# Kernel optimization log

Hardware: AMD Instinct MI355X
Metric: run time of the kernel (lower is better)

## Reference

```python
import jax, jax.numpy as jnp
import numpy as np
from jax import lax

TOP_N = 4
CAT_NUM = 4
IOU_THRESH = 0.25
PAD = 224
OUT_SZ = 224


def _gen_edge_anchors():
    # Faithful port of NTSNet._generate_default_anchor_maps for 448x448 input.
    settings = (
        dict(stride=32, size=48, scale=[2 ** (1.0 / 3.0), 2 ** (2.0 / 3.0)], ar=[0.667, 1, 1.5]),
        dict(stride=64, size=96, scale=[2 ** (1.0 / 3.0), 2 ** (2.0 / 3.0)], ar=[0.667, 1, 1.5]),
        dict(stride=128, size=192, scale=[1, 2 ** (1.0 / 3.0), 2 ** (2.0 / 3.0)], ar=[0.667, 1, 1.5]),
    )
    inp = np.array([448, 448], dtype=np.float32)
    edges = []
    for s in settings:
        stride = s['stride']
        oh, ow = np.ceil(inp / stride).astype(int)
        ostart = stride / 2.0
        oy = np.arange(ostart, ostart + stride * oh, stride, dtype=np.float32).reshape(oh, 1)
        ox = np.arange(ostart, ostart + stride * ow, stride, dtype=np.float32).reshape(1, ow)
        cy = np.broadcast_to(oy, (oh, ow)); cx = np.broadcast_to(ox, (oh, ow))
        for sc in s['scale']:
            for ar in s['ar']:
                h = s['size'] * sc / float(ar) ** 0.5
                w = s['size'] * sc * float(ar) ** 0.5
                e = np.stack([cy - h / 2.0, cx - w / 2.0, cy + h / 2.0, cx + w / 2.0], axis=-1).reshape(-1, 4)
                edges.append(e)
    return np.concatenate(edges, 0).astype(np.float32)

EDGE_ANCHORS = (_gen_edge_anchors() + PAD).astype(np.int32)  # [1614,4] (y0,x0,y1,x1) in padded coords
BOXES_F = jnp.asarray(EDGE_ANCHORS, jnp.float32)
BOXES_I = jnp.asarray(EDGE_ANCHORS, jnp.int32)
AREAS = (BOXES_F[:, 2] - BOXES_F[:, 0]) * (BOXES_F[:, 3] - BOXES_F[:, 1])
N_ANCHORS = EDGE_ANCHORS.shape[0]  # 1614


def _nms_single(scores):
    # Greedy hard NMS: pick top score, suppress IoU >= thresh, repeat TOP_N times.
    def step(valid, _):
        s = jnp.where(valid, scores, -jnp.inf)
        i = jnp.argmax(s)
        b = BOXES_F[i]
        sy = jnp.maximum(BOXES_F[:, 0], b[0]); sx = jnp.maximum(BOXES_F[:, 1], b[1])
        ey = jnp.minimum(BOXES_F[:, 2], b[2]); ex = jnp.minimum(BOXES_F[:, 3], b[3])
        ly = ey - sy; lx = ex - sx
        inter = jnp.where((ly < 0) | (lx < 0), 0.0, ly * lx)
        iou = inter / (AREAS + AREAS[i] - inter)
        return valid & (iou < IOU_THRESH), i
    _, idx = lax.scan(step, jnp.ones((N_ANCHORS,), bool), None, length=TOP_N)
    return idx  # [TOP_N] int


def _crop_resize(img, box):
    # img: [3, 896, 896]; box: int [4] = (y0,x0,y1,x1); bilinear, align_corners=True -> [3,224,224]
    hmax = img.shape[-1] - 1
    y0, x0, y1, x1 = box[0], box[1], box[2], box[3]
    t = jnp.arange(OUT_SZ, dtype=jnp.float32) / (OUT_SZ - 1.0)
    ys = y0.astype(jnp.float32) + t * (y1 - y0 - 1).astype(jnp.float32)
    xs = x0.astype(jnp.float32) + t * (x1 - x0 - 1).astype(jnp.float32)
    yf = jnp.floor(ys); xf = jnp.floor(xs)
    wy = (ys - yf)[None, :, None]; wx = (xs - xf)[None, None, :]
    yl = yf.astype(jnp.int32); yh = jnp.minimum(yl + 1, hmax)
    xl = xf.astype(jnp.int32); xh = jnp.minimum(xl + 1, hmax)
    g = lambda yi, xi: img[:, yi[:, None], xi[None, :]]
    top = g(yl, xl) * (1.0 - wx) + g(yl, xh) * wx
    bot = g(yh, xl) * (1.0 - wx) + g(yh, xh) * wx
    return top * (1.0 - wy) + bot * wy


def _conv(x, w, b, stride, pad):
    y = lax.conv_general_dilated(x, w, (stride, stride), ((pad, pad), (pad, pad)),
                                 dimension_numbers=('NCHW', 'OIHW', 'NCHW'))
    return y + b[None, :, None, None]


def _forward(x, bb_w, bb_b, w1, b1, t1w, t1b, w2, b2, t2w, t2b, w3, b3, t3w, t3b, cw, cb):
    B = x.shape[0]
    backbone = lambda z: jax.nn.relu(_conv(z, bb_w, bb_b, 32, 0))
    raw_pre = backbone(x)  # [B,2048,14,14]
    # Navigator unit
    y1 = jax.nn.relu(_conv(raw_pre, w1, b1, 1, 1))                                  # [B,128,14,14]
    z1 = (jnp.einsum('bchw,oc->bohw', y1, t1w) + t1b[None, :, None, None]).reshape(B, -1)
    y2 = jax.nn.relu(_conv(y1, w2, b2, 2, 1))                                        # [B,128,7,7]
    z2 = (jnp.einsum('bchw,oc->bohw', y2, t2w) + t2b[None, :, None, None]).reshape(B, -1)
    y3 = jax.nn.relu(_conv(y2, w3, b3, 2, 1))                                        # [B,128,4,4]
    z3 = (jnp.einsum('bchw,oc->bohw', y3, t3w) + t3b[None, :, None, None]).reshape(B, -1)
    rpn_score = jnp.concatenate([z1, z2, z3], axis=1)  # [B,1614]
    top_idx = jax.vmap(_nms_single)(rpn_score)          # [B,TOP_N]
    boxes = BOXES_I[top_idx]                            # [B,TOP_N,4]
    x_pad = jnp.pad(x, ((0, 0), (0, 0), (PAD, PAD), (PAD, PAD)))  # [B,3,896,896]
    parts = jax.vmap(lambda img, bs: jax.vmap(lambda b: _crop_resize(img, b))(bs))(x_pad, boxes)
    parts = lax.stop_gradient(parts).reshape(B * TOP_N, 3, OUT_SZ, OUT_SZ)  # .detach() in torch
    part_feat = backbone(parts).mean(axis=(2, 3)).reshape(B, TOP_N, 2048)
    part_feat = part_feat[:, :CAT_NUM].reshape(B, -1)   # [B,8192]
    raw_feat = lax.stop_gradient(raw_pre).mean(axis=(2, 3))  # [B,2048] (detached in torch)
    concat = jnp.concatenate([part_feat, raw_feat], axis=1)  # [B,10240]
    return concat @ cw.T + cb                           # [B,200]


def setup_inputs() -> dict:
    key = jax.random.key(0)
    ks = jax.random.split(key, 12)
    def w(k, shape, fan_in):
        return jax.random.normal(k, shape, jnp.float32) * np.float32(np.sqrt(2.0 / fan_in))
    return {
        'x': jax.random.normal(ks[0], (8, 3, 448, 448), jnp.float32),
        'bb_w': w(ks[1], (2048, 3, 32, 32), 3 * 32 * 32), 'bb_b': jnp.zeros((2048,), jnp.float32),
        'w1': w(ks[2], (128, 2048, 3, 3), 2048 * 9), 'b1': jnp.zeros((128,), jnp.float32),
        't1w': w(ks[3], (6, 128), 128), 't1b': jnp.zeros((6,), jnp.float32),
        'w2': w(ks[4], (128, 128, 3, 3), 128 * 9), 'b2': jnp.zeros((128,), jnp.float32),
        't2w': w(ks[5], (6, 128), 128), 't2b': jnp.zeros((6,), jnp.float32),
        'w3': w(ks[6], (128, 128, 3, 3), 128 * 9), 'b3': jnp.zeros((128,), jnp.float32),
        't3w': w(ks[7], (9, 128), 128), 't3b': jnp.zeros((9,), jnp.float32),
        'cw': w(ks[8], (200, 2048 * (CAT_NUM + 1)), 2048 * (CAT_NUM + 1)),
        'cb': jnp.zeros((200,), jnp.float32),
    }


def reference(x, bb_w, bb_b, w1, b1, t1w, t1b, w2, b2, t2w, t2b, w3, b3, t3w, t3b, cw, cb):
    return _forward(x, bb_w, bb_b, w1, b1, t1w, t1b, w2, b2, t2w, t2b, w3, b3, t3w, t3b, cw, cb)
```

## Files before the change

### kernel.cpp

```cpp
#include <hip/hip_runtime.h>
#include <math.h>


typedef _Float16 h8 __attribute__((ext_vector_type(8)));
typedef float f32x4 __attribute__((ext_vector_type(4)));

#define ASCALE 256.0f
#define WSCALE 16384.0f
#define RSCALE (1.0f / (256.0f * 16384.0f))
#define PSLAB ((size_t)1664 * 2048)

__device__ __forceinline__ void gload16(const void* g, void* l) {
  __builtin_amdgcn_global_load_lds(
      (__attribute__((address_space(1))) void*)(void*)(uintptr_t)g,
      (__attribute__((address_space(3))) void*)l, 16, 0, 0);
}

__device__ void anchors_body(int i, int* anch, float* areas) {
  if (i >= 1614) return;
  int stride, oh, a, pos;
  double size, sc;
  const double C13 = 1.2599210498948732;
  const double C23 = 1.5874010519681994;
  if (i < 1176) {
    stride = 32; size = 48.0; oh = 14; a = i / 196; pos = i % 196;
    sc = (a / 3 == 0) ? C13 : C23;
  } else if (i < 1470) {
    int r = i - 1176; stride = 64; size = 96.0; oh = 7; a = r / 49; pos = r % 49;
    sc = (a / 3 == 0) ? C13 : C23;
  } else {
    int r = i - 1470; stride = 128; size = 192.0; oh = 4; a = r / 16; pos = r % 16;
    int si = a / 3;
    sc = (si == 0) ? 1.0 : ((si == 1) ? C13 : C23);
  }
  int ari = a % 3;
  double ar = (ari == 0) ? 0.667 : ((ari == 1) ? 1.0 : 1.5);
  int gy = pos / oh, gx = pos % oh;
  float cy = 0.5f * (float)stride + (float)(stride * gy);
  float cx = 0.5f * (float)stride + (float)(stride * gx);
  double ss = sqrt(ar);
  double hd = (size * sc) / ss;
  double wd = (size * sc) * ss;
  float hh = (float)(hd * 0.5), wh = (float)(wd * 0.5);
  int y0 = (int)((cy - hh) + 224.0f), x0 = (int)((cx - wh) + 224.0f);
  int y1i = (int)((cy + hh) + 224.0f), x1i = (int)((cx + wh) + 224.0f);
  anch[i * 4 + 0] = y0; anch[i * 4 + 1] = x0;
  anch[i * 4 + 2] = y1i; anch[i * 4 + 3] = x1i;
  areas[i] = (float)(y1i - y0) * (float)(x1i - x0);
}

__global__ __launch_bounds__(256) void prep_small(int* __restrict__ anch,
                                                  float* __restrict__ areas,
                                                  const float* __restrict__ w2,
                                                  float* __restrict__ w2p,
                                                  const float* __restrict__ w3,
                                                  float* __restrict__ w3p) {
  int b = blockIdx.x, t = threadIdx.x;
  if (b < 7) { anchors_body(b * 256 + t, anch, areas); return; }
  const float* src; float* dst; int idx;
  if (b < 7 + 576) { src = w2; dst = w2p; idx = (b - 7) * 256 + t; }
  else             { src = w3; dst = w3p; idx = (b - 583) * 256 + t; }
  if (idx >= 128 * 9 * 128) return;
  int c = idx % 128; int r2 = idx / 128; int tap = r2 % 9; int o = r2 / 9;
  dst[idx] = src[(o * 128 + c) * 9 + tap];
}

__global__ __launch_bounds__(256) void split_w(const float* __restrict__ src,
                                               _Float16* __restrict__ h,
                                               _Float16* __restrict__ l, int n8) {
  int i = blockIdx.x * 256 + threadIdx.x;
  if (i >= n8) return;
  float4 v0 = *(const float4*)(src + (size_t)i * 8);
  float4 v1 = *(const float4*)(src + (size_t)i * 8 + 4);
  float vv[8] = {v0.x, v0.y, v0.z, v0.w, v1.x, v1.y, v1.z, v1.w};
  h8 vh, vl;
#pragma unroll
  for (int j = 0; j < 8; ++j) {
    float s = vv[j] * WSCALE;
    _Float16 a = (_Float16)s;
    vh[j] = a; vl[j] = (_Float16)(s - (float)a);
  }
  *(h8*)(h + (size_t)i * 8) = vh;
  *(h8*)(l + (size_t)i * 8) = vl;
}

__global__ __launch_bounds__(256) void split_w1(const float* __restrict__ w1,
                                                _Float16* __restrict__ h,
                                                _Float16* __restrict__ l) {
  __shared__ float buf[4608];
  int o = blockIdx.x >> 2, ct = (blockIdx.x & 3) * 512;
  const float* src = w1 + (size_t)o * 18432 + (size_t)ct * 9;
  for (int i = threadIdx.x; i < 4608; i += 256) buf[i] = src[i];
  __syncthreads();
  for (int i = threadIdx.x; i < 4608; i += 256) {
    int tap = i / 512, c = i - tap * 512;
    float v = buf[c * 9 + tap] * WSCALE;
    _Float16 a = (_Float16)v;
    size_t o2 = ((size_t)o * 9 + tap) * 2048 + ct + c;
    h[o2] = a; l[o2] = (_Float16)(v - (float)a);
  }
}

__global__ __launch_bounds__(256) void split_x(const float* __restrict__ x,
                                               _Float16* __restrict__ Ah,
                                               _Float16* __restrict__ Al) {
  int i = blockIdx.x * 256 + threadIdx.x;
  if (i >= 1664 * 384) return;
  int kq = i % 384, m = i / 384;
  int k = kq * 8;
  h8 vh = {}, vl = {};
  if (m < 1568) {
    int b = m / 196, pos = m % 196;
    int c = k >> 10, r = (k >> 5) & 31, col = k & 31;
    int py = (pos / 14) * 32 + r, px = (pos % 14) * 32 + col;
    const float* sp2 = x + (((size_t)(b * 3 + c) * 448 + py) * 448 + px);
    float4 v0 = *(const float4*)sp2;
    float4 v1 = *(const float4*)(sp2 + 4);
    float vv[8] = {v0.x, v0.y, v0.z, v0.w, v1.x, v1.y, v1.z, v1.w};
#pragma unroll
    for (int j = 0; j < 8; ++j) {
      float s = vv[j] * ASCALE;
      _Float16 a = (_Float16)s;
      vh[j] = a; vl[j] = (_Float16)(s - (float)a);
    }
  }
  *(h8*)(Ah + (size_t)m * 3072 + k) = vh;
  *(h8*)(Al + (size_t)m * 3072 + k) = vl;
}

__global__ __launch_bounds__(256) void gemm_bb_mfma(
    const _Float16* __restrict__ Ah, const _Float16* __restrict__ Al,
    const _Float16* __restrict__ Bh, const _Float16* __restrict__ Bl,
    float* __restrict__ P) {
  __shared__ __align__(16) char lds[65536];
  const int t = threadIdx.x;
  const int bid = blockIdx.x + 13 * blockIdx.y;
  const int r = bid >> 3;
  const int m0 = (r >> 1) * 128;
  const int n0 = ((bid & 7) * 2 + (r & 1)) * 128;
  const int kz = blockIdx.z;
  const int lane = t & 63, w = t >> 6;
  const int wm = (w >> 1) * 64, wn = (w & 1) * 64;
  const int lrow = lane & 15, kg = lane >> 4;

  int offA[4], offB[4];
#pragma unroll
  for (int i = 0; i < 4; ++i) {
    int ba = (wm + i * 16 + lrow) * 64 + kg * 16;
    offA[i] = ba ^ (((ba >> 7) & 3) << 4);
    int bb2 = (wn + i * 16 + lrow) * 64 + kg * 16;
    offB[i] = bb2 ^ (((bb2 >> 7) & 3) << 4);
  }
  size_t gAo[2], gBo[2];
  int ldso[2];
#pragma unroll
  for (int e = 0; e < 2; ++e) {
    int p = e * 256 + t;
    int lsl = p ^ ((p >> 3) & 3);
    int row = lsl >> 2, kq = lsl & 3;
    gAo[e] = (size_t)(m0 + row) * 3072 + kq * 8;
    gBo[e] = (size_t)(n0 + row) * 3072 + kq * 8;
    ldso[e] = e * 4096 + (t & 192) * 16;
  }

  auto STAGE = [&](int buf, int k0) {
    char* L = lds + buf * 32768;
#pragma unroll
    for (int e = 0; e < 2; ++e) {
      gload16(Ah + gAo[e] + k0, L + ldso[e]);
      gload16(Al + gAo[e] + k0, L + 8192 + ldso[e]);
      gload16(Bh + gBo[e] + k0, L + 16384 + ldso[e]);
      gload16(Bl + gBo[e] + k0, L + 24576 + ldso[e]);
    }
  };

  f32x4 acc[4][4] = {};
  const int kbeg = kz * 1536, kend = kbeg + 1536;
  STAGE(0, kbeg);
  __syncthreads();
  int cur = 0;
  for (int k0 = kbeg; k0 < kend; k0 += 32) {
    if (k0 + 32 < kend) STAGE(cur ^ 1, k0 + 32);
    const char* L = lds + cur * 32768;
    h8 fah[4], fal[4], fbh[4], fbl[4];
#pragma unroll
    for (int i = 0; i < 4; ++i) {
      fah[i] = *(const h8*)(L + offA[i]);
      fal[i] = *(const h8*)(L + 8192 + offA[i]);
      fbh[i] = *(const h8*)(L + 16384 + offB[i]);
      fbl[i] = *(const h8*)(L + 24576 + offB[i]);
    }
#pragma unroll
    for (int i = 0; i < 4; ++i)
#pragma unroll
      for (int j = 0; j < 4; ++j)
        acc[i][j] = __builtin_amdgcn_mfma_f32_16x16x32_f16(fah[i], fbh[j], acc[i][j], 0, 0, 0);
#pragma unroll
    for (int i = 0; i < 4; ++i)
#pragma unroll
      for (int j = 0; j < 4; ++j)
        acc[i][j] = __builtin_amdgcn_mfma_f32_16x16x32_f16(fah[i], fbl[j], acc[i][j], 0, 0, 0);
#pragma unroll
    for (int i = 0; i < 4; ++i)
#pragma unroll
      for (int j = 0; j < 4; ++j)
        acc[i][j] = __builtin_amdgcn_mfma_f32_16x16x32_f16(fal[i], fbh[j], acc[i][j], 0, 0, 0);
    __syncthreads();
    cur ^= 1;
  }
  float* Pz = P + (size_t)kz * PSLAB;
  const int prow = (lane >> 4) * 4;
#pragma unroll
  for (int i = 0; i < 4; ++i) {
#pragma unroll
    for (int j = 0; j < 4; ++j) {
      int n = n0 + wn + j * 16 + lrow;
#pragma unroll
      for (int r2 = 0; r2 < 4; ++r2) {
        int m = m0 + wm + i * 16 + prow + r2;
        Pz[(size_t)m * 2048 + n] = acc[i][j][r2];
      }
    }
  }
}

__global__ __launch_bounds__(256) void bb_reduce_split(const float* __restrict__ P,
                                                       const float* __restrict__ bias,
                                                       _Float16* __restrict__ h,
                                                       _Float16* __restrict__ l) {
  int idx = blockIdx.x * 256 + threadIdx.x;
  int m = idx >> 8, col = (idx & 255) * 8;
  if (m >= 1664) return;
  size_t o = (size_t)m * 2048 + col;
  if (m >= 1568) {
    h8 z = {};
    *(h8*)(h + o) = z;
    *(h8*)(l + o) = z;
    return;
  }
  h8 vh, vl;
#pragma unroll
  for (int q = 0; q < 2; ++q) {
    float4 s0 = *(const float4*)(P + o + q * 4);
    float4 s1 = *(const float4*)(P + PSLAB + o + q * 4);
    float4 b = *(const float4*)(bias + col + q * 4);
    float v[4];
    v[0] = fmaxf(fmaf(s0.x + s1.x, RSCALE, b.x), 0.f);
    v[1] = fmaxf(fmaf(s0.y + s1.y, RSCALE, b.y), 0.f);
    v[2] = fmaxf(fmaf(s0.z + s1.z, RSCALE, b.z), 0.f);
    v[3] = fmaxf(fmaf(s0.w + s1.w, RSCALE, b.w), 0.f);
#pragma unroll
    for (int j = 0; j < 4; ++j) {
      float s = v[j] * ASCALE;
      _Float16 a = (_Float16)s;
      vh[q * 4 + j] = a; vl[q * 4 + j] = (_Float16)(s - (float)a);
    }
  }
  *(h8*)(h + o) = vh;
  *(h8*)(l + o) = vl;
}

__global__ __launch_bounds__(256) void feat_reduce(const float* __restrict__ P,
                                                   const float* __restrict__ bias,
                                                   float* __restrict__ out,
                                                   int rows) {
  int g = blockIdx.x >> 5, chunk = blockIdx.x & 31;
  int col = chunk * 64 + (threadIdx.x & 63), rl = threadIdx.x >> 6;
  const float* base0 = P + ((size_t)g * rows) * 2048 + col;
  const float* base1 = base0 + PSLAB;
  float bcol = bias[col];
  float s = 0.f;
  for (int r = rl; r < rows; r += 4)
    s += fmaxf(fmaf(base0[(size_t)r * 2048] + base1[(size_t)r * 2048], RSCALE, bcol), 0.f);
  __shared__ float red[4][64];
  red[rl][threadIdx.x & 63] = s;
  __syncthreads();
  if (rl == 0) {
    int c = threadIdx.x & 63;
    out[(size_t)g * 2048 + col] =
        ((red[0][c] + red[1][c]) + (red[2][c] + red[3][c])) / (float)rows;
  }
}

__global__ __launch_bounds__(256) void gemm_nav_mfma(
    const _Float16* __restrict__ Ah, const _Float16* __restrict__ Al,
    const _Float16* __restrict__ Bh, const _Float16* __restrict__ Bl,
    float* __restrict__ part) {
  __shared__ __align__(16) char lds[65536];
  const int t = threadIdx.x;
  const int bid = blockIdx.x + 13 * blockIdx.y;
  const int orig = (bid & 7) * 52 + (bid >> 3);
  const int m0 = (orig % 13) * 128;
  const int sp = orig / 13;
  const int lane = t & 63, w = t >> 6;
  const int wm = (w >> 1) * 64, wn = (w & 1) * 64;
  const int lrow = lane & 15, kg = lane >> 4;

  int offA[4], offB[4];
#pragma unroll
  for (int i = 0; i < 4; ++i) {
    int ba = (wm + i * 16 + lrow) * 64 + kg * 16;
    offA[i] = ba ^ (((ba >> 7) & 3) << 4);
    int bb2 = (wn + i * 16 + lrow) * 64 + kg * 16;
    offB[i] = bb2 ^ (((bb2 >> 7) & 3) << 4);
  }
  size_t gBo[2];
  int ldso[2], akq8[2], ab[2], apy[2], apx[2], amv[2];
#pragma unroll
  for (int e = 0; e < 2; ++e) {
    int p = e * 256 + t;
    int lsl = p ^ ((p >> 3) & 3);
    int row = lsl >> 2, kq = lsl & 3;
    gBo[e] = (size_t)row * 18432 + kq * 8;
    ldso[e] = e * 4096 + (t & 192) * 16;
    int m = m0 + row;
    amv[e] = (m < 1568);
    int b = m / 196, pos = m % 196;
    ab[e] = b; apy[e] = pos / 14; apx[e] = pos % 14;
    akq8[e] = kq * 8;
  }

  auto STAGE = [&](int buf, int k0) {
    const int tap = k0 >> 11;
    const int c = k0 & 2047;
    const int dy = tap / 3 - 1, dx = tap % 3 - 1;
    char* L = lds + buf * 32768;
#pragma unroll
    for (int e = 0; e < 2; ++e) {
      int sy = apy[e] + dy, sx = apx[e] + dx;
      bool ok = amv[e] && ((unsigned)sy < 14u) && ((unsigned)sx < 14u);
      size_t rowi = ok ? (size_t)(ab[e] * 196 + sy * 14 + sx) : (size_t)1600;
      size_t ao = rowi * 2048 + c + akq8[e];
      gload16(Ah + ao, L + ldso[e]);
      gload16(Al + ao, L + 8192 + ldso[e]);
      gload16(Bh + gBo[e] + k0, L + 16384 + ldso[e]);
      gload16(Bl + gBo[e] + k0, L + 24576 + ldso[e]);
    }
  };

  f32x4 acc[4][4] = {};
  const int kbeg = sp * 576, kend = kbeg + 576;
  STAGE(0, kbeg);
  __syncthreads();
  int cur = 0;
  for (int k0 = kbeg; k0 < kend; k0 += 32) {
    if (k0 + 32 < kend) STAGE(cur ^ 1, k0 + 32);
    const char* L = lds + cur * 32768;
    h8 fah[4], fal[4], fbh[4], fbl[4];
#pragma unroll
    for (int i = 0; i < 4; ++i) {
      fah[i] = *(const h8*)(L + offA[i]);
      fal[i] = *(const h8*)(L + 8192 + offA[i]);
      fbh[i] = *(const h8*)(L + 16384 + offB[i]);
      fbl[i] = *(const h8*)(L + 24576 + offB[i]);
    }
#pragma unroll
    for (int i = 0; i < 4; ++i)
#pragma unroll
      for (int j = 0; j < 4; ++j)
        acc[i][j] = __builtin_amdgcn_mfma_f32_16x16x32_f16(fah[i], fbh[j], acc[i][j], 0, 0, 0);
#pragma unroll
    for (int i = 0; i < 4; ++i)
#pragma unroll
      for (int j = 0; j < 4; ++j)
        acc[i][j] = __builtin_amdgcn_mfma_f32_16x16x32_f16(fah[i], fbl[j], acc[i][j], 0, 0, 0);
#pragma unroll
    for (int i = 0; i < 4; ++i)
#pragma unroll
      for (int j = 0; j < 4; ++j)
        acc[i][j] = __builtin_amdgcn_mfma_f32_16x16x32_f16(fal[i], fbh[j], acc[i][j], 0, 0, 0);
    __syncthreads();
    cur ^= 1;
  }
  const int prow = (lane >> 4) * 4;
#pragma unroll
  for (int i = 0; i < 4; ++i) {
#pragma unroll
    for (int j = 0; j < 4; ++j) {
      int n = wn + j * 16 + lrow;
#pragma unroll
      for (int r = 0; r < 4; ++r) {
        int m = m0 + wm + i * 16 + prow + r;
        if (m < 1568)
          part[((size_t)sp * 1568 + m) * 128 + n] = acc[i][j][r] * RSCALE;
      }
    }
  }
}

__global__ __launch_bounds__(256) void y1_reduce(const float* __restrict__ part,
                                                 const float* __restrict__ b1,
                                                 float* __restrict__ y1) {
  int idx = blockIdx.x * 256 + threadIdx.x;
  if (idx >= 1568 * 32) return;
  int o = (idx * 4) & 127;
  float4 s = *(const float4*)(b1 + o);
#pragma unroll
  for (int sp = 0; sp < 32; ++sp) {
    float4 v = *(const float4*)(part + (size_t)sp * 1568 * 128 + (size_t)idx * 4);
    s.x += v.x; s.y += v.y; s.z += v.z; s.w += v.w;
  }
  s.x = fmaxf(s.x, 0.f); s.y = fmaxf(s.y, 0.f);
  s.z = fmaxf(s.z, 0.f); s.w = fmaxf(s.w, 0.f);
  *(float4*)(y1 + (size_t)idx * 4) = s;
}

__global__ __launch_bounds__(256) void conv3x3s2(const float* __restrict__ in,
                                                 const float* __restrict__ wp,
                                                 const float* __restrict__ bias,
                                                 float* __restrict__ out,
                                                 int Hin, int Hout) {
  int idx = blockIdx.x * 256 + threadIdx.x;
  int total = 8 * Hout * Hout * 128;
  if (idx >= total) return;
  int o = idx & 127; int pos = idx >> 7;
  int ox = pos % Hout; int t2 = pos / Hout; int oy = t2 % Hout; int b = t2 / Hout;
  float acc = bias[o];
  for (int dy = 0; dy < 3; ++dy) {
    int iy = 2 * oy - 1 + dy;
    if (iy < 0 || iy >= Hin) continue;
    for (int dx = 0; dx < 3; ++dx) {
      int ix = 2 * ox - 1 + dx;
      if (ix < 0 || ix >= Hin) continue;
      const float* ip = in + ((b * Hin + iy) * Hin + ix) * 128;
      const float* wgt = wp + (o * 9 + dy * 3 + dx) * 128;
#pragma unroll 4
      for (int c = 0; c < 128; c += 4) {
        float4 a = *(const float4*)(ip + c);
        float4 ww = *(const float4*)(wgt + c);
        acc += a.x * ww.x + a.y * ww.y + a.z * ww.z + a.w * ww.w;
      }
    }
  }
  out[idx] = fmaxf(acc, 0.f);
}

__global__ __launch_bounds__(256) void scores_kernel(
    const float* __restrict__ y1, const float* __restrict__ y2,
    const float* __restrict__ y3, const float* __restrict__ t1w,
    const float* __restrict__ t1b, const float* __restrict__ t2w,
    const float* __restrict__ t2b, const float* __restrict__ t3w,
    const float* __restrict__ t3b, float* __restrict__ scores) {
  int idx = blockIdx.x * 256 + threadIdx.x;
  if (idx >= 8 * 1614) return;
  int b = idx / 1614, sI = idx % 1614;
  const float* f; const float* w; float bias;
  if (sI < 1176) {
    int a = sI / 196;
    f = y1 + (b * 196 + (sI % 196)) * 128; w = t1w + a * 128; bias = t1b[a];
  } else if (sI < 1470) {
    int r = sI - 1176; int a = r / 49;
    f = y2 + (b * 49 + (r % 49)) * 128; w = t2w + a * 128; bias = t2b[a];
  } else {
    int r = sI - 1470; int a = r / 16;
    f = y3 + (b * 16 + (r % 16)) * 128; w = t3w + a * 128; bias = t3b[a];
  }
  float acc = 0.f;
  for (int c = 0; c < 128; c += 4) {
    float4 a4 = *(const float4*)(f + c);
    float4 w4 = *(const float4*)(w + c);
    acc += a4.x * w4.x + a4.y * w4.y + a4.z * w4.z + a4.w * w4.w;
  }
  scores[idx] = acc + bias;
}

__global__ __launch_bounds__(256) void nms_kernel(const float* __restrict__ scores,
                                                  const int* __restrict__ anch,
                                                  const float* __restrict__ areas,
                                                  int* __restrict__ boxes) {
  const int b = blockIdx.x, t = threadIdx.x;
  const int lane = t & 63, wid = t >> 6;
  const float* s = scores + b * 1614;
  __shared__ unsigned char valid[1614];
  __shared__ float wv[4];
  __shared__ int wi[4];
  __shared__ int ssel;
  for (int i = t; i < 1614; i += 256) valid[i] = 1;
  __syncthreads();
  for (int n = 0; n < 4; ++n) {
    float best = -INFINITY; int bi = 0x7fffffff;
    for (int i = t; i < 1614; i += 256) {
      if (valid[i]) {
        float v = s[i];
        if (v > best || (v == best && i < bi)) { best = v; bi = i; }
      }
    }
#pragma unroll
    for (int off = 32; off > 0; off >>= 1) {
      float ov = __shfl_down(best, off, 64);
      int oi = __shfl_down(bi, off, 64);
      if (ov > best || (ov == best && oi < bi)) { best = ov; bi = oi; }
    }
    if (lane == 0) { wv[wid] = best; wi[wid] = bi; }
    __syncthreads();
    if (t == 0) {
      float bv = wv[0]; int bj = wi[0];
#pragma unroll
      for (int q = 1; q < 4; ++q)
        if (wv[q] > bv || (wv[q] == bv && wi[q] < bj)) { bv = wv[q]; bj = wi[q]; }
      if (bj > 1613) bj = 0;
      ssel = bj;
      ((int4*)boxes)[b * 4 + n] = ((const int4*)anch)[bj];
    }
    __syncthreads();
    int sel = ssel;
    const int4 bb = ((const int4*)anch)[sel];
    const float Ai = areas[sel];
    for (int i = t; i < 1614; i += 256) {
      if (!valid[i]) continue;
      const int4 ab = ((const int4*)anch)[i];
      float sy = fmaxf((float)ab.x, (float)bb.x);
      float sx = fmaxf((float)ab.y, (float)bb.y);
      float ey = fminf((float)ab.z, (float)bb.z);
      float ex = fminf((float)ab.w, (float)bb.w);
      float ly = ey - sy, lx = ex - sx;
      float inter = (ly < 0.f || lx < 0.f) ? 0.f : ly * lx;
      float iou = inter / (areas[i] + Ai - inter);
      if (iou >= 0.25f) valid[i] = 0;
    }
    __syncthreads();
  }
}

__global__ __launch_bounds__(256) void crop_kernel(const float* __restrict__ x,
                                                   const int* __restrict__ boxes,
                                                   _Float16* __restrict__ Ah,
                                                   _Float16* __restrict__ Al) {
  int idx = blockIdx.x * 256 + threadIdx.x;
  if (idx >= 32 * 3 * 224 * 28) return;
  int pxq = idx % 28; int t1 = idx / 28; int py = t1 % 224; int t2 = t1 / 224;
  int c = t2 % 3; int p = t2 / 3;
  int b = p >> 2;
  int px0 = pxq * 8;
  const int4 bb = ((const int4*)boxes)[p];
  float ty = (float)py / 223.0f;
  float ys = (float)bb.x + ty * (float)(bb.z - bb.x - 1);
  float yf = floorf(ys);
  float wy = ys - yf;
  int yl = (int)yf;
  int yh = min(yl + 1, 895);
  const float* img = x + (size_t)(b * 3 + c) * 448 * 448;
  auto samp = [&](int yy, int xx) -> float {
    yy -= 224; xx -= 224;
    if (yy < 0 || yy >= 448 || xx < 0 || xx >= 448) return 0.f;
    return img[yy * 448 + xx];
  };
  h8 vh, vl;
#pragma unroll
  for (int q = 0; q < 8; ++q) {
    int px = px0 + q;
    float txf = (float)px / 223.0f;
    float xs = (float)bb.y + txf * (float)(bb.w - bb.y - 1);
    float xf = floorf(xs);
    float wx = xs - xf;
    int xl = (int)xf;
    int xh = min(xl + 1, 895);
    float v00 = samp(yl, xl), v01 = samp(yl, xh);
    float v10 = samp(yh, xl), v11 = samp(yh, xh);
    float top = v00 * (1.f - wx) + v01 * wx;
    float bot = v10 * (1.f - wx) + v11 * wx;
    float val = top * (1.f - wy) + bot * wy;
    float sv = val * ASCALE;
    _Float16 a = (_Float16)sv;
    vh[q] = a; vl[q] = (_Float16)(sv - (float)a);
  }
  int i = py >> 5, r = py & 31, j = px0 >> 5, col = px0 & 31;
  int m = p * 49 + i * 7 + j;
  int k = (c << 10) + (r << 5) + col;
  *(h8*)(Ah + (size_t)m * 3072 + k) = vh;
  *(h8*)(Al + (size_t)m * 3072 + k) = vl;
}

__global__ __launch_bounds__(256) void final_kernel(const float* __restrict__ pfeat,
                                                    const float* __restrict__ rfeat,
                                                    const float* __restrict__ cw,
                                                    const float* __restrict__ cb,
                                                    float* __restrict__ out) {
  int gw = (blockIdx.x * 256 + threadIdx.x) >> 6;
  int lane = threadIdx.x & 63;
  if (gw >= 1600) return;
  int b = gw / 200, j = gw % 200;
  const float* wr = cw + (size_t)j * 10240;
  const float* pf = pfeat + (size_t)b * 8192;
  float acc = 0.f;
  for (int k = lane * 4; k < 8192; k += 256) {
    float4 a = *(const float4*)(pf + k);
    float4 w = *(const float4*)(wr + k);
    acc += a.x * w.x + a.y * w.y + a.z * w.z + a.w * w.w;
  }
  const float* rf = rfeat + (size_t)b * 2048;
  const float* wr2 = wr + 8192;
  for (int k = lane * 4; k < 2048; k += 256) {
    float4 a = *(const float4*)(rf + k);
    float4 w = *(const float4*)(wr2 + k);
    acc += a.x * w.x + a.y * w.y + a.z * w.z + a.w * w.w;
  }
#pragma unroll
  for (int off = 32; off > 0; off >>= 1) acc += __shfl_down(acc, off, 64);
  if (lane == 0) out[b * 200 + j] = acc + cb[j];
}

extern "C" void kernel_launch(void* const* d_in, const int* in_sizes, int n_in,
                              void* d_out, int out_size, void* d_ws, size_t ws_size,
                              hipStream_t stream) {
  const float* x   = (const float*)d_in[0];
  const float* bbw = (const float*)d_in[1];
  const float* bbb = (const float*)d_in[2];
  const float* w1  = (const float*)d_in[3];
  const float* b1  = (const float*)d_in[4];
  const float* t1w = (const float*)d_in[5];
  const float* t1b = (const float*)d_in[6];
  const float* w2  = (const float*)d_in[7];
  const float* b2  = (const float*)d_in[8];
  const float* t2w = (const float*)d_in[9];
  const float* t2b = (const float*)d_in[10];
  const float* w3  = (const float*)d_in[11];
  const float* b3  = (const float*)d_in[12];
  const float* t3w = (const float*)d_in[13];
  const float* t3b = (const float*)d_in[14];
  const float* cw  = (const float*)d_in[15];
  const float* cb  = (const float*)d_in[16];
  float* out = (float*)d_out;

  char* p = (char*)d_ws;
  auto alloc = [&](size_t bytes) -> char* {
    char* r = p; p += (bytes + 255) & ~(size_t)255; return r;
  };
  int*      anch  = (int*)     alloc((size_t)1614 * 4 * 4);
  float*    areas = (float*)   alloc((size_t)1614 * 4);
  _Float16* bWh   = (_Float16*)alloc((size_t)2048 * 3072 * 2);
  _Float16* bWl   = (_Float16*)alloc((size_t)2048 * 3072 * 2);
  _Float16* w1h   = (_Float16*)alloc((size_t)128 * 18432 * 2);
  _Float16* w1l   = (_Float16*)alloc((size_t)128 * 18432 * 2);
  _Float16* Ahh   = (_Float16*)alloc((size_t)1664 * 3072 * 2);
  _Float16* All   = (_Float16*)alloc((size_t)1664 * 3072 * 2);
  _Float16* rawh  = (_Float16*)alloc((size_t)1664 * 2048 * 2);
  _Float16* rawl  = (_Float16*)alloc((size_t)1664 * 2048 * 2);
  float*    w2p   = (float*)   alloc((size_t)128 * 9 * 128 * 4);
  float*    w3p   = (float*)   alloc((size_t)128 * 9 * 128 * 4);
  char*     big   = alloc((size_t)2 * PSLAB * 4);
  float*    Pbuf  = (float*)big;
  float*    y1s   = (float*)big;
  float*    y1v   = (float*)   alloc((size_t)1568 * 128 * 4);
  float*    y2v   = (float*)   alloc((size_t)392 * 128 * 4);
  float*    y3v   = (float*)   alloc((size_t)128 * 128 * 4);
  float*    sc    = (float*)   alloc((size_t)8 * 1614 * 4);
  int*      boxes = (int*)     alloc((size_t)8 * 4 * 4 * 4);
  float*    pfeat = (float*)   alloc((size_t)32 * 2048 * 4);
  float*    rfeat = (float*)   alloc((size_t)8 * 2048 * 4);

  prep_small<<<7 + 576 + 576, 256, 0, stream>>>(anch, areas, w2, w2p, w3, w3p);
  split_w<<<(2048 * 3072 / 8 + 255) / 256, 256, 0, stream>>>(bbw, bWh, bWl, 2048 * 3072 / 8);
  split_w1<<<512, 256, 0, stream>>>(w1, w1h, w1l);
  split_x<<<(1664 * 384 + 255) / 256, 256, 0, stream>>>(x, Ahh, All);

  gemm_bb_mfma<<<dim3(13, 16, 2), 256, 0, stream>>>(Ahh, All, bWh, bWl, Pbuf);
  bb_reduce_split<<<1664, 256, 0, stream>>>(Pbuf, bbb, rawh, rawl);
  feat_reduce<<<8 * 32, 256, 0, stream>>>(Pbuf, bbb, rfeat, 196);
  gemm_nav_mfma<<<dim3(13, 32), 256, 0, stream>>>(rawh, rawl, w1h, w1l, y1s);
  y1_reduce<<<(1568 * 32 + 255) / 256, 256, 0, stream>>>(y1s, b1, y1v);
  conv3x3s2<<<(8 * 7 * 7 * 128 + 255) / 256, 256, 0, stream>>>(y1v, w2p, b2, y2v, 14, 7);
  conv3x3s2<<<(8 * 4 * 4 * 128 + 255) / 256, 256, 0, stream>>>(y2v, w3p, b3, y3v, 7, 4);
  scores_kernel<<<(8 * 1614 + 255) / 256, 256, 0, stream>>>(
      y1v, y2v, y3v, t1w, t1b, t2w, t2b, t3w, t3b, sc);
  nms_kernel<<<8, 256, 0, stream>>>(sc, anch, areas, boxes);
  crop_kernel<<<(32 * 3 * 224 * 28 + 255) / 256, 256, 0, stream>>>(x, boxes, Ahh, All);
  gemm_bb_mfma<<<dim3(13, 16, 2), 256, 0, stream>>>(Ahh, All, bWh, bWl, Pbuf);
  feat_reduce<<<32 * 32, 256, 0, stream>>>(Pbuf, bbb, pfeat, 49);
  final_kernel<<<400, 256, 0, stream>>>(pfeat, rfeat, cw, cb, out);
}
```

Measured before the change: 371.8 us.

## Merge prep kernels, fuse backbone reduce with feature pooling, retile nav GEMM

New measurement: 363.3 us, median of 2. -2.3%, faster.

```diff
diff --git a/kernel.cpp b/kernel.cpp
--- a/kernel.cpp
+++ b/kernel.cpp
@@ -49,83 +49,79 @@
   areas[i] = (float)(y1i - y0) * (float)(x1i - x0);
 }
 
-__global__ __launch_bounds__(256) void prep_small(int* __restrict__ anch,
-                                                  float* __restrict__ areas,
-                                                  const float* __restrict__ w2,
-                                                  float* __restrict__ w2p,
-                                                  const float* __restrict__ w3,
-                                                  float* __restrict__ w3p) {
+__global__ __launch_bounds__(256) void mega_prep(
+    int* __restrict__ anch, float* __restrict__ areas,
+    const float* __restrict__ w2, float* __restrict__ w2p,
+    const float* __restrict__ w3, float* __restrict__ w3p,
+    const float* __restrict__ bbw, _Float16* __restrict__ bWh, _Float16* __restrict__ bWl,
+    const float* __restrict__ w1, _Float16* __restrict__ w1h, _Float16* __restrict__ w1l,
+    const float* __restrict__ x, _Float16* __restrict__ Ah, _Float16* __restrict__ Al) {
+  __shared__ float buf[4608];
   int b = blockIdx.x, t = threadIdx.x;
   if (b < 7) { anchors_body(b * 256 + t, anch, areas); return; }
-  const float* src; float* dst; int idx;
-  if (b < 7 + 576) { src = w2; dst = w2p; idx = (b - 7) * 256 + t; }
-  else             { src = w3; dst = w3p; idx = (b - 583) * 256 + t; }
-  if (idx >= 128 * 9 * 128) return;
-  int c = idx % 128; int r2 = idx / 128; int tap = r2 % 9; int o = r2 / 9;
-  dst[idx] = src[(o * 128 + c) * 9 + tap];
-}
-
-__global__ __launch_bounds__(256) void split_w(const float* __restrict__ src,
-                                               _Float16* __restrict__ h,
-                                               _Float16* __restrict__ l, int n8) {
-  int i = blockIdx.x * 256 + threadIdx.x;
-  if (i >= n8) return;
-  float4 v0 = *(const float4*)(src + (size_t)i * 8);
-  float4 v1 = *(const float4*)(src + (size_t)i * 8 + 4);
-  float vv[8] = {v0.x, v0.y, v0.z, v0.w, v1.x, v1.y, v1.z, v1.w};
-  h8 vh, vl;
-#pragma unroll
-  for (int j = 0; j < 8; ++j) {
-    float s = vv[j] * WSCALE;
-    _Float16 a = (_Float16)s;
-    vh[j] = a; vl[j] = (_Float16)(s - (float)a);
-  }
-  *(h8*)(h + (size_t)i * 8) = vh;
-  *(h8*)(l + (size_t)i * 8) = vl;
-}
-
-__global__ __launch_bounds__(256) void split_w1(const float* __restrict__ w1,
-                                                _Float16* __restrict__ h,
-                                                _Float16* __restrict__ l) {
-  __shared__ float buf[4608];
-  int o = blockIdx.x >> 2, ct = (blockIdx.x & 3) * 512;
-  const float* src = w1 + (size_t)o * 18432 + (size_t)ct * 9;
-  for (int i = threadIdx.x; i < 4608; i += 256) buf[i] = src[i];
-  __syncthreads();
-  for (int i = threadIdx.x; i < 4608; i += 256) {
-    int tap = i / 512, c = i - tap * 512;
-    float v = buf[c * 9 + tap] * WSCALE;
-    _Float16 a = (_Float16)v;
-    size_t o2 = ((size_t)o * 9 + tap) * 2048 + ct + c;
-    h[o2] = a; l[o2] = (_Float16)(v - (float)a);
-  }
-}
-
-__global__ __launch_bounds__(256) void split_x(const float* __restrict__ x,
-                                               _Float16* __restrict__ Ah,
-                                               _Float16* __restrict__ Al) {
-  int i = blockIdx.x * 256 + threadIdx.x;
-  if (i >= 1664 * 384) return;
-  int kq = i % 384, m = i / 384;
-  int k = kq * 8;
-  h8 vh = {}, vl = {};
-  if (m < 1568) {
-    int b = m / 196, pos = m % 196;
-    int c = k >> 10, r = (k >> 5) & 31, col = k & 31;
-    int py = (pos / 14) * 32 + r, px = (pos % 14) * 32 + col;
-    const float* sp2 = x + (((size_t)(b * 3 + c) * 448 + py) * 448 + px);
-    float4 v0 = *(const float4*)sp2;
-    float4 v1 = *(const float4*)(sp2 + 4);
+  if (b < 1159) {
+    const float* src; float* dst; int idx;
+    if (b < 583) { src = w2; dst = w2p; idx = (b - 7) * 256 + t; }
+    else         { src = w3; dst = w3p; idx = (b - 583) * 256 + t; }
+    if (idx >= 128 * 9 * 128) return;
+    int c = idx % 128; int r2 = idx / 128; int tap = r2 % 9; int o = r2 / 9;
+    dst[idx] = src[(o * 128 + c) * 9 + tap];
+    return;
+  }
+  if (b < 4231) {
+    int i = (b - 1159) * 256 + t;
+    float4 v0 = *(const float4*)(bbw + (size_t)i * 8);
+    float4 v1 = *(const float4*)(bbw + (size_t)i * 8 + 4);
     float vv[8] = {v0.x, v0.y, v0.z, v0.w, v1.x, v1.y, v1.z, v1.w};
+    h8 vh, vl;
 #pragma unroll
     for (int j = 0; j < 8; ++j) {
-      float s = vv[j] * ASCALE;
+      float s = vv[j] * WSCALE;
       _Float16 a = (_Float16)s;
       vh[j] = a; vl[j] = (_Float16)(s - (float)a);
     }
-  }
-  *(h8*)(Ah + (size_t)m * 3072 + k) = vh;
-  *(h8*)(Al + (size_t)m * 3072 + k) = vl;
+    *(h8*)(bWh + (size_t)i * 8) = vh;
+    *(h8*)(bWl + (size_t)i * 8) = vl;
+    return;
+  }
+  if (b < 4743) {
+    int bb = b - 4231;
+    int o = bb >> 2, ct = (bb & 3) * 512;
+    const float* src = w1 + (size_t)o * 18432 + (size_t)ct * 9;
+    for (int i = t; i < 4608; i += 256) buf[i] = src[i];
+    __syncthreads();
+    for (int i = t; i < 4608; i += 256) {
+      int tap = i / 512, c = i - tap * 512;
+      float v = buf[c * 9 + tap] * WSCALE;
+      _Float16 a = (_Float16)v;
+      size_t o2 = ((size_t)o * 9 + tap) * 2048 + ct + c;
+      w1h[o2] = a; w1l[o2] = (_Float16)(v - (float)a);
+    }
+    return;
+  }
+  {
+    int i = (b - 4743) * 256 + t;
+    int kq = i % 384, m = i / 384;
+    int k = kq * 8;
+    h8 vh = {}, vl = {};
+    if (m < 1568) {
+      int bb = m / 196, pos = m % 196;
+      int c = k >> 10, r = (k >> 5) & 31, col = k & 31;
+      int py = (pos / 14) * 32 + r, px = (pos % 14) * 32 + col;
+      const float* sp2 = x + (((size_t)(bb * 3 + c) * 448 + py) * 448 + px);
+      float4 v0 = *(const float4*)sp2;
+      float4 v1 = *(const float4*)(sp2 + 4);
+      float vv[8] = {v0.x, v0.y, v0.z, v0.w, v1.x, v1.y, v1.z, v1.w};
+#pragma unroll
+      for (int j = 0; j < 8; ++j) {
+        float s = vv[j] * ASCALE;
+        _Float16 a = (_Float16)s;
+        vh[j] = a; vl[j] = (_Float16)(s - (float)a);
+      }
+    }
+    *(h8*)(Ah + (size_t)m * 3072 + k) = vh;
+    *(h8*)(Al + (size_t)m * 3072 + k) = vl;
+  }
 }
 
 __global__ __launch_bounds__(256) void gemm_bb_mfma(
@@ -224,40 +220,43 @@
   }
 }
 
-__global__ __launch_bounds__(256) void bb_reduce_split(const float* __restrict__ P,
-                                                       const float* __restrict__ bias,
-                                                       _Float16* __restrict__ h,
-                                                       _Float16* __restrict__ l) {
-  int idx = blockIdx.x * 256 + threadIdx.x;
-  int m = idx >> 8, col = (idx & 255) * 8;
-  if (m >= 1664) return;
-  size_t o = (size_t)m * 2048 + col;
-  if (m >= 1568) {
-    h8 z = {};
-    *(h8*)(h + o) = z;
-    *(h8*)(l + o) = z;
+__global__ __launch_bounds__(256) void nav_prep(const float* __restrict__ P,
+                                                const float* __restrict__ bias,
+                                                _Float16* __restrict__ h,
+                                                _Float16* __restrict__ l,
+                                                float* __restrict__ rfeat) {
+  int b = blockIdx.x, t = threadIdx.x;
+  if (b >= 256) {
+    int b2 = b - 256;
+    for (int i = t; i < 24 * 256; i += 256) {
+      int row = 1568 + b2 * 24 + (i >> 8);
+      int colq = (i & 255) * 8;
+      h8 z = {};
+      *(h8*)(h + (size_t)row * 2048 + colq) = z;
+      *(h8*)(l + (size_t)row * 2048 + colq) = z;
+    }
     return;
   }
-  h8 vh, vl;
-#pragma unroll
-  for (int q = 0; q < 2; ++q) {
-    float4 s0 = *(const float4*)(P + o + q * 4);
-    float4 s1 = *(const float4*)(P + PSLAB + o + q * 4);
-    float4 b = *(const float4*)(bias + col + q * 4);
-    float v[4];
-    v[0] = fmaxf(fmaf(s0.x + s1.x, RSCALE, b.x), 0.f);
-    v[1] = fmaxf(fmaf(s0.y + s1.y, RSCALE, b.y), 0.f);
-    v[2] = fmaxf(fmaf(s0.z + s1.z, RSCALE, b.z), 0.f);
-    v[3] = fmaxf(fmaf(s0.w + s1.w, RSCALE, b.w), 0.f);
-#pragma unroll
-    for (int j = 0; j < 4; ++j) {
-      float s = v[j] * ASCALE;
-      _Float16 a = (_Float16)s;
-      vh[q * 4 + j] = a; vl[q * 4 + j] = (_Float16)(s - (float)a);
-    }
-  }
-  *(h8*)(h + o) = vh;
-  *(h8*)(l + o) = vl;
+  int g = b >> 5, chunk = b & 31;
+  int col = chunk * 64 + (t & 63), rl = t >> 6;
+  float bcol = bias[col];
+  float s = 0.f;
+  for (int r = rl; r < 196; r += 4) {
+    size_t o = ((size_t)(g * 196 + r)) * 2048 + col;
+    float v = fmaxf(fmaf(P[o] + P[PSLAB + o], RSCALE, bcol), 0.f);
+    s += v;
+    float sv = v * ASCALE;
+    _Float16 a = (_Float16)sv;
+    h[o] = a; l[o] = (_Float16)(sv - (float)a);
+  }
+  __shared__ float red[4][64];
+  red[rl][t & 63] = s;
+  __syncthreads();
+  if (rl == 0) {
+    int c = t & 63;
+    rfeat[(size_t)g * 2048 + col] =
+        ((red[0][c] + red[1][c]) + (red[2][c] + red[3][c])) / 196.0f;
+  }
 }
 
 __global__ __launch_bounds__(256) void feat_reduce(const float* __restrict__ P,
@@ -286,86 +285,95 @@
     const _Float16* __restrict__ Ah, const _Float16* __restrict__ Al,
     const _Float16* __restrict__ Bh, const _Float16* __restrict__ Bl,
     float* __restrict__ part) {
-  __shared__ __align__(16) char lds[65536];
+  __shared__ __align__(16) char lds[49152];
   const int t = threadIdx.x;
-  const int bid = blockIdx.x + 13 * blockIdx.y;
-  const int orig = (bid & 7) * 52 + (bid >> 3);
-  const int m0 = (orig % 13) * 128;
-  const int sp = orig / 13;
+  const int bid = blockIdx.x;
+  const int orig = (bid & 7) * 50 + (bid >> 3);
+  const int m0 = (orig % 25) * 64;
+  const int sp = orig / 25;
   const int lane = t & 63, w = t >> 6;
-  const int wm = (w >> 1) * 64, wn = (w & 1) * 64;
+  const int wm = (w >> 1) * 32, wn = (w & 1) * 64;
   const int lrow = lane & 15, kg = lane >> 4;
 
-  int offA[4], offB[4];
-#pragma unroll
-  for (int i = 0; i < 4; ++i) {
+  int offA[2], offB[4];
+#pragma unroll
+  for (int i = 0; i < 2; ++i) {
     int ba = (wm + i * 16 + lrow) * 64 + kg * 16;
     offA[i] = ba ^ (((ba >> 7) & 3) << 4);
+  }
+#pragma unroll
+  for (int i = 0; i < 4; ++i) {
     int bb2 = (wn + i * 16 + lrow) * 64 + kg * 16;
     offB[i] = bb2 ^ (((bb2 >> 7) & 3) << 4);
   }
+  int lslA = t ^ ((t >> 3) & 3);
+  int rowA = lslA >> 2, kqA = lslA & 3;
+  int mA = m0 + rowA;
+  int amv = (mA < 1568);
+  int ab = mA / 196, aps = mA % 196;
+  int apy = aps / 14, apx = aps % 14;
+  int akq8 = kqA * 8;
+  int ldsoA = (t & 192) * 16;
   size_t gBo[2];
-  int ldso[2], akq8[2], ab[2], apy[2], apx[2], amv[2];
+  int ldsoB[2];
 #pragma unroll
   for (int e = 0; e < 2; ++e) {
     int p = e * 256 + t;
     int lsl = p ^ ((p >> 3) & 3);
     int row = lsl >> 2, kq = lsl & 3;
     gBo[e] = (size_t)row * 18432 + kq * 8;
-    ldso[e] = e * 4096 + (t & 192) * 16;
-    int m = m0 + row;
-    amv[e] = (m < 1568);
-    int b = m / 196, pos = m % 196;
-    ab[e] = b; apy[e] = pos / 14; apx[e] = pos % 14;
-    akq8[e] = kq * 8;
+    ldsoB[e] = e * 4096 + (t & 192) * 16;
   }
 
   auto STAGE = [&](int buf, int k0) {
     const int tap = k0 >> 11;
     const int c = k0 & 2047;
     const int dy = tap / 3 - 1, dx = tap % 3 - 1;
-    char* L = lds + buf * 32768;
+    char* L = lds + buf * 24576;
+    int sy = apy + dy, sx = apx + dx;
+    bool ok = amv && ((unsigned)sy < 14u) && ((unsigned)sx < 14u);
+    size_t rowi = ok ? (size_t)(ab * 196 + sy * 14 + sx) : (size_t)1600;
+    size_t ao = rowi * 2048 + c + akq8;
+    gload16(Ah + ao, L + ldsoA);
+    gload16(Al + ao, L + 4096 + ldsoA);
 #pragma unroll
     for (int e = 0; e < 2; ++e) {
-      int sy = apy[e] + dy, sx = apx[e] + dx;
-      bool ok = amv[e] && ((unsigned)sy < 14u) && ((unsigned)sx < 14u);
-      size_t rowi = ok ? (size_t)(ab[e] * 196 + sy * 14 + sx) : (size_t)1600;
-      size_t ao = rowi * 2048 + c + akq8[e];
-      gload16(Ah + ao, L + ldso[e]);
-      gload16(Al + ao, L + 8192 + ldso[e]);
-      gload16(Bh + gBo[e] + k0, L + 16384 + ldso[e]);
-      gload16(Bl + gBo[e] + k0, L + 24576 + ldso[e]);
+      gload16(Bh + gBo[e] + k0, L + 8192 + ldsoB[e]);
+      gload16(Bl + gBo[e] + k0, L + 16384 + ldsoB[e]);
     }
   };
 
-  f32x4 acc[4][4] = {};
-  const int kbeg = sp * 576, kend = kbeg + 576;
+  f32x4 acc[2][4] = {};
+  const int kbeg = sp * 1152, kend = kbeg + 1152;
   STAGE(0, kbeg);
   __syncthreads();
   int cur = 0;
   for (int k0 = kbeg; k0 < kend; k0 += 32) {
     if (k0 + 32 < kend) STAGE(cur ^ 1, k0 + 32);
-    const char* L = lds + cur * 32768;
-    h8 fah[4], fal[4], fbh[4], fbl[4];
-#pragma unroll
-    for (int i = 0; i < 4; ++i) {
+    const char* L = lds + cur * 24576;
+    h8 fah[2], fal[2], fbh[4], fbl[4];
+#pragma unroll
+    for (int i = 0; i < 2; ++i) {
       fah[i] = *(const h8*)(L + offA[i]);
-      fal[i] = *(const h8*)(L + 8192 + offA[i]);
-      fbh[i] = *(const h8*)(L + 16384 + offB[i]);
-      fbl[i] = *(const h8*)(L + 24576 + offB[i]);
-    }
-#pragma unroll
-    for (int i = 0; i < 4; ++i)
+      fal[i] = *(const h8*)(L + 4096 + offA[i]);
+    }
+#pragma unroll
+    for (int j = 0; j < 4; ++j) {
+      fbh[j] = *(const h8*)(L + 8192 + offB[j]);
+      fbl[j] = *(const h8*)(L + 16384 + offB[j]);
+    }
+#pragma unroll
+    for (int i = 0; i < 2; ++i)
 #pragma unroll
       for (int j = 0; j < 4; ++j)
         acc[i][j] = __builtin_amdgcn_mfma_f32_16x16x32_f16(fah[i], fbh[j], acc[i][j], 0, 0, 0);
 #pragma unroll
-    for (int i = 0; i < 4; ++i)
+    for (int i = 0; i < 2; ++i)
 #pragma unroll
       for (int j = 0; j < 4; ++j)
         acc[i][j] = __builtin_amdgcn_mfma_f32_16x16x32_f16(fah[i], fbl[j], acc[i][j], 0, 0, 0);
 #pragma unroll
-    for (int i = 0; i < 4; ++i)
+    for (int i = 0; i < 2; ++i)
 #pragma unroll
       for (int j = 0; j < 4; ++j)
         acc[i][j] = __builtin_amdgcn_mfma_f32_16x16x32_f16(fal[i], fbh[j], acc[i][j], 0, 0, 0);
@@ -374,7 +382,7 @@
   }
   const int prow = (lane >> 4) * 4;
 #pragma unroll
-  for (int i = 0; i < 4; ++i) {
+  for (int i = 0; i < 2; ++i) {
 #pragma unroll
     for (int j = 0; j < 4; ++j) {
       int n = wn + j * 16 + lrow;
@@ -396,7 +404,7 @@
   int o = (idx * 4) & 127;
   float4 s = *(const float4*)(b1 + o);
 #pragma unroll
-  for (int sp = 0; sp < 32; ++sp) {
+  for (int sp = 0; sp < 16; ++sp) {
     float4 v = *(const float4*)(part + (size_t)sp * 1568 * 128 + (size_t)idx * 4);
     s.x += v.x; s.y += v.y; s.z += v.z; s.w += v.w;
   }
@@ -649,15 +657,12 @@
   float*    pfeat = (float*)   alloc((size_t)32 * 2048 * 4);
   float*    rfeat = (float*)   alloc((size_t)8 * 2048 * 4);
 
-  prep_small<<<7 + 576 + 576, 256, 0, stream>>>(anch, areas, w2, w2p, w3, w3p);
-  split_w<<<(2048 * 3072 / 8 + 255) / 256, 256, 0, stream>>>(bbw, bWh, bWl, 2048 * 3072 / 8);
-  split_w1<<<512, 256, 0, stream>>>(w1, w1h, w1l);
-  split_x<<<(1664 * 384 + 255) / 256, 256, 0, stream>>>(x, Ahh, All);
+  mega_prep<<<7239, 256, 0, stream>>>(anch, areas, w2, w2p, w3, w3p,
+                                      bbw, bWh, bWl, w1, w1h, w1l, x, Ahh, All);
 
   gemm_bb_mfma<<<dim3(13, 16, 2), 256, 0, stream>>>(Ahh, All, bWh, bWl, Pbuf);
-  bb_reduce_split<<<1664, 256, 0, stream>>>(Pbuf, bbb, rawh, rawl);
-  feat_reduce<<<8 * 32, 256, 0, stream>>>(Pbuf, bbb, rfeat, 196);
-  gemm_nav_mfma<<<dim3(13, 32), 256, 0, stream>>>(rawh, rawl, w1h, w1l, y1s);
+  nav_prep<<<260, 256, 0, stream>>>(Pbuf, bbb, rawh, rawl, rfeat);
+  gemm_nav_mfma<<<400, 256, 0, stream>>>(rawh, rawl, w1h, w1l, y1s);
   y1_reduce<<<(1568 * 32 + 255) / 256, 256, 0, stream>>>(y1s, b1, y1v);
   conv3x3s2<<<(8 * 7 * 7 * 128 + 255) / 256, 256, 0, stream>>>(y1v, w2p, b2, y2v, 14, 7);
   conv3x3s2<<<(8 * 4 * 4 * 128 + 255) / 256, 256, 0, stream>>>(y2v, w3p, b3, y3v, 7, 4);
```
